# Performance work log

Hardware: AMD Instinct MI355X
Metric: run time of the kernel (lower is better)

## Reference

```python
import jax, jax.numpy as jnp
import numpy as np

BATCH, N_IN, N_OUT, D = 32768, 256, 256, 8

def setup_inputs() -> dict:
    key = jax.random.key(0)
    k1, k2 = jax.random.split(key)
    noise_std = 1.0 / (N_IN * (D + 1))
    x = jax.random.normal(k1, (BATCH, N_IN), dtype=jnp.float32)
    c_basis = noise_std * jax.random.normal(k2, (N_OUT, N_IN, D + 1), dtype=jnp.float32)
    c_act = jnp.ones((N_OUT, N_IN), dtype=jnp.float32)
    return {"x": x, "c_basis": c_basis, "c_act": c_act}

def _cheby_basis(x, degree):
    # x: (batch, n_in) -> (batch, n_in, degree+1) Chebyshev T_k(tanh(x))
    t = jnp.tanh(x)
    polys = [jnp.ones_like(t), t]
    for _ in range(2, degree + 1):
        polys.append(2.0 * t * polys[-1] - polys[-2])
    return jnp.stack(polys[: degree + 1], axis=-1)

def reference(x, c_basis, c_act):
    batch = x.shape[0]
    n_out = c_basis.shape[0]
    degree = c_basis.shape[-1] - 1
    Ti = _cheby_basis(x, degree)                      # (batch, n_in, D+1)
    cheb = Ti.reshape(batch, -1)                      # (batch, n_in*(D+1))
    cheb_w = (c_basis * c_act[..., None]).reshape(n_out, -1)
    return jnp.matmul(cheb, cheb_w.T)                 # (batch, n_out)
```

## Files before the change

### kernel.cpp

```cpp
#include <hip/hip_runtime.h>
#include <hip/hip_bf16.h>

#define BATCH 32768
#define NIN   256
#define NOUT  256

typedef __attribute__((ext_vector_type(8))) short bf16x8;
typedef __attribute__((ext_vector_type(4))) float f32x4;
typedef __attribute__((ext_vector_type(2))) float f32x2;
typedef __attribute__((ext_vector_type(4))) unsigned int u32x4;

static __device__ __forceinline__ unsigned short bf16_rne(float f) {
  unsigned u = __float_as_uint(f);
  u += 0x7fffu + ((u >> 16) & 1u);
  return (unsigned short)(u >> 16);
}

static __device__ __forceinline__ float fast_tanh(float v) {
  float a = fabsf(v);
  float z = __expf(-2.0f * a);
  float r = (1.0f - z) * __builtin_amdgcn_rcpf(1.0f + z);
  return copysignf(r, v);
}

static __device__ __forceinline__ unsigned pack_pair(f32x2 v) {
  __hip_bfloat162 h2 = __float22bfloat162_rn(make_float2(v[0], v[1]));
  union { __hip_bfloat162 h; unsigned u; } cv;
  cv.h = h2;
  return cv.u;
}

__global__ void cheby_prepack(const float* __restrict__ cb,
                              const float* __restrict__ ca,
                              unsigned short* __restrict__ Bp) {
  int tid = blockIdx.x * 256 + threadIdx.x;
  int j    = tid & 7;
  int col  = (tid >> 3) & 15;
  int kg   = (tid >> 7) & 3;
  int tile = (tid >> 9) & 15;
  int ic   = (tid >> 13) & 7;
  int dm   = tid >> 16;
  int i = ic * 32 + kg * 8 + j;
  int n = tile * 16 + col;
  float w = cb[n * (NIN * 9) + i * 9 + (dm + 1)] * ca[n * NIN + i];
  Bp[tid] = bf16_rne(w);
}

__global__ void cheby_bias(const float* __restrict__ cb,
                           const float* __restrict__ ca,
                           float* __restrict__ bias) {
  int n = blockIdx.x;
  int l = threadIdx.x;
  float s = 0.0f;
  #pragma unroll
  for (int k = 0; k < 4; ++k) {
    int i = l + k * 64;
    s += cb[n * (NIN * 9) + i * 9] * ca[n * NIN + i];
  }
  #pragma unroll
  for (int off = 32; off; off >>= 1) s += __shfl_down(s, off);
  if (l == 0) bias[n] = s;
}

__global__ __launch_bounds__(256, 2)
void cheby_mfma(const float* __restrict__ x,
                const unsigned short* __restrict__ Bp,
                const float* __restrict__ bias,
                float* __restrict__ out) {
  __shared__ unsigned short Asm[2][8][4][512];

  int tid  = threadIdx.x;
  int w    = tid >> 6;
  int lane = tid & 63;
  int row16 = lane & 15;
  int kg    = lane >> 4;

  int base_row = blockIdx.x * 64;
  int tile0    = w * 4;

  int wrow = tid >> 2;
  int wfg  = tid & 3;
  const float* xw = x + (size_t)(base_row + wrow) * NIN + wfg * 8;
  char* wbase = (char*)&Asm[0][0][wrow >> 4][0] + (wfg * 256 + (wrow & 15) * 16);

  const char* bp_lane = (const char*)Bp + kg * 256 + row16 * 16;
  const char* abase   = (const char*)&Asm[0][0][0][0] + lane * 16;

  f32x4 acc[4][4];
  #pragma unroll
  for (int a = 0; a < 4; ++a)
    #pragma unroll
    for (int b = 0; b < 4; ++b) acc[a][b] = (f32x4)0.0f;

  f32x4 xa = *(const f32x4*)xw;
  f32x4 xb = *(const f32x4*)(xw + 4);

  for (int ic = 0; ic < 8; ++ic) {
    int buf = ic & 1;
    f32x2 cur[4], prev[4], t2[4];
    #pragma unroll
    for (int p = 0; p < 4; ++p) {
      float va = (p < 2) ? xa[2 * p]     : xb[2 * p - 4];
      float vb = (p < 2) ? xa[2 * p + 1] : xb[2 * p - 3];
      float ta = fast_tanh(va);
      float tb = fast_tanh(vb);
      cur[p]  = (f32x2){ta, tb};
      t2[p]   = cur[p] + cur[p];
      prev[p] = (f32x2){1.0f, 1.0f};
    }
    char* wp = wbase + buf * 32768;
    #pragma unroll
    for (int d = 1; d <= 8; ++d) {
      u32x4 pk;
      #pragma unroll
      for (int p = 0; p < 4; ++p) pk[p] = pack_pair(cur[p]);
      *(u32x4*)(wp + (d - 1) * 4096) = pk;
      if (d < 8) {
        #pragma unroll
        for (int p = 0; p < 4; ++p) {
          f32x2 nx = __builtin_elementwise_fma(t2[p], cur[p], -prev[p]);
          prev[p] = cur[p];
          cur[p]  = nx;
        }
      }
    }
    if (ic < 7) {
      xa = *(const f32x4*)(xw + (ic + 1) * 32);
      xb = *(const f32x4*)(xw + (ic + 1) * 32 + 4);
    }
    __syncthreads();

    const char* bpi = bp_lane + (size_t)(ic * 16 + tile0) * 1024;
    const char* ai  = abase + buf * 32768;
    bf16x8 bcur[4], acur[4];
    #pragma unroll
    for (int nt = 0; nt < 4; ++nt)
      bcur[nt] = *(const bf16x8*)(bpi + nt * 1024);
    #pragma unroll
    for (int mt = 0; mt < 4; ++mt)
      acur[mt] = *(const bf16x8*)(ai + mt * 1024);

    #pragma unroll
    for (int d = 1; d <= 8; ++d) {
      bf16x8 bnxt[4], anxt[4];
      if (d < 8) {
        #pragma unroll
        for (int nt = 0; nt < 4; ++nt)
          bnxt[nt] = *(const bf16x8*)(bpi + (size_t)d * 131072 + nt * 1024);
        #pragma unroll
        for (int mt = 0; mt < 4; ++mt)
          anxt[mt] = *(const bf16x8*)(ai + (d * 4 + mt) * 1024);
      }
      #pragma unroll
      for (int mt = 0; mt < 4; ++mt)
        #pragma unroll
        for (int nt = 0; nt < 4; ++nt)
          acc[mt][nt] = __builtin_amdgcn_mfma_f32_16x16x32_bf16(
              acur[mt], bcur[nt], acc[mt][nt], 0, 0, 0);
      if (d < 8) {
        #pragma unroll
        for (int nt = 0; nt < 4; ++nt) bcur[nt] = bnxt[nt];
        #pragma unroll
        for (int mt = 0; mt < 4; ++mt) acur[mt] = anxt[mt];
      }
    }
  }

  #pragma unroll
  for (int nt = 0; nt < 4; ++nt) {
    int c = (tile0 + nt) * 16 + row16;
    float bv = bias[c];
    #pragma unroll
    for (int mt = 0; mt < 4; ++mt) {
      int r0 = base_row + mt * 16 + kg * 4;
      #pragma unroll
      for (int q = 0; q < 4; ++q)
        out[(size_t)(r0 + q) * NOUT + c] = acc[mt][nt][q] + bv;
    }
  }
}

extern "C" void kernel_launch(void* const* d_in, const int* in_sizes, int n_in,
                              void* d_out, int out_size, void* d_ws, size_t ws_size,
                              hipStream_t stream) {
  const float* x  = (const float*)d_in[0];
  const float* cb = (const float*)d_in[1];
  const float* ca = (const float*)d_in[2];
  float* out = (float*)d_out;

  unsigned short* Bp = (unsigned short*)d_ws;
  float* bias = (float*)((char*)d_ws + 8 * NIN * NOUT * 2);

  cheby_prepack<<<(8 * NIN * NOUT) / 256, 256, 0, stream>>>(cb, ca, Bp);
  cheby_bias<<<NOUT, 64, 0, stream>>>(cb, ca, bias);
  cheby_mfma<<<512, 256, 0, stream>>>(x, Bp, bias, out);
}
```

Baseline: 52.23 us.

## Software-pipeline Chebyshev basis generation with MFMA over double-buffered LDS

Restructures the main loop so that the Chebyshev basis for chunk ic+1 is computed and written into the alternate LDS buffer while MFMAs consume chunk ic, with a prologue and epilogue around the loop. This lets VALU transcendental and pack work overlap the matrix core work instead of running serially before each barrier. It also changes the LDS write mapping so each wave writes its own 16-row slice, and it drops explicit register double-buffering of fragments in favour of per-step loads. The cost is higher register pressure from carrying the recurrence state alongside the accumulators and fragments.

```diff
diff --git a/kernel.cpp b/kernel.cpp
--- a/kernel.cpp
+++ b/kernel.cpp
@@ -28,6 +28,21 @@
   union { __hip_bfloat162 h; unsigned u; } cv;
   cv.h = h2;
   return cv.u;
+}
+
+static __device__ __forceinline__ void init_state(const f32x4 x0, const f32x4 x1,
+                                                  f32x2* cur, f32x2* prev,
+                                                  f32x2* t2) {
+  #pragma unroll
+  for (int p = 0; p < 4; ++p) {
+    float va = (p < 2) ? x0[2 * p]     : x1[2 * p - 4];
+    float vb = (p < 2) ? x0[2 * p + 1] : x1[2 * p - 3];
+    float ta = fast_tanh(va);
+    float tb = fast_tanh(vb);
+    cur[p]  = (f32x2){ta, tb};
+    t2[p]   = cur[p] + cur[p];
+    prev[p] = (f32x2){1.0f, 1.0f};
+  }
 }
 
 __global__ void cheby_prepack(const float* __restrict__ cb,
@@ -78,13 +93,10 @@
   int base_row = blockIdx.x * 64;
   int tile0    = w * 4;
 
-  int wrow = tid >> 2;
-  int wfg  = tid & 3;
-  const float* xw = x + (size_t)(base_row + wrow) * NIN + wfg * 8;
-  char* wbase = (char*)&Asm[0][0][wrow >> 4][0] + (wfg * 256 + (wrow & 15) * 16);
-
+  const float* xw = x + (size_t)(base_row + w * 16 + row16) * NIN + kg * 8;
+  char* wbase = (char*)Asm + (w * 1024 + lane * 16);
+  const char* abase   = (const char*)Asm + lane * 16;
   const char* bp_lane = (const char*)Bp + kg * 256 + row16 * 16;
-  const char* abase   = (const char*)&Asm[0][0][0][0] + lane * 16;
 
   f32x4 acc[4][4];
   #pragma unroll
@@ -94,27 +106,15 @@
 
   f32x4 xa = *(const f32x4*)xw;
   f32x4 xb = *(const f32x4*)(xw + 4);
-
-  for (int ic = 0; ic < 8; ++ic) {
-    int buf = ic & 1;
+  {
     f32x2 cur[4], prev[4], t2[4];
-    #pragma unroll
-    for (int p = 0; p < 4; ++p) {
-      float va = (p < 2) ? xa[2 * p]     : xb[2 * p - 4];
-      float vb = (p < 2) ? xa[2 * p + 1] : xb[2 * p - 3];
-      float ta = fast_tanh(va);
-      float tb = fast_tanh(vb);
-      cur[p]  = (f32x2){ta, tb};
-      t2[p]   = cur[p] + cur[p];
-      prev[p] = (f32x2){1.0f, 1.0f};
-    }
-    char* wp = wbase + buf * 32768;
+    init_state(xa, xb, cur, prev, t2);
     #pragma unroll
     for (int d = 1; d <= 8; ++d) {
       u32x4 pk;
       #pragma unroll
       for (int p = 0; p < 4; ++p) pk[p] = pack_pair(cur[p]);
-      *(u32x4*)(wp + (d - 1) * 4096) = pk;
+      *(u32x4*)(wbase + (d - 1) * 4096) = pk;
       if (d < 8) {
         #pragma unroll
         for (int p = 0; p < 4; ++p) {
@@ -124,45 +124,72 @@
         }
       }
     }
-    if (ic < 7) {
-      xa = *(const f32x4*)(xw + (ic + 1) * 32);
-      xb = *(const f32x4*)(xw + (ic + 1) * 32 + 4);
-    }
-    __syncthreads();
-
+  }
+  xa = *(const f32x4*)(xw + 32);
+  xb = *(const f32x4*)(xw + 36);
+  __syncthreads();
+
+  for (int ic = 0; ic < 7; ++ic) {
+    int buf = ic & 1;
+    f32x2 cur[4], prev[4], t2[4];
+    init_state(xa, xb, cur, prev, t2);
+    if (ic < 6) {
+      xa = *(const f32x4*)(xw + (ic + 2) * 32);
+      xb = *(const f32x4*)(xw + (ic + 2) * 32 + 4);
+    }
+    const char* ai  = abase + buf * 32768;
+    char*       wp  = wbase + (buf ^ 1) * 32768;
     const char* bpi = bp_lane + (size_t)(ic * 16 + tile0) * 1024;
-    const char* ai  = abase + buf * 32768;
-    bf16x8 bcur[4], acur[4];
-    #pragma unroll
-    for (int nt = 0; nt < 4; ++nt)
-      bcur[nt] = *(const bf16x8*)(bpi + nt * 1024);
-    #pragma unroll
-    for (int mt = 0; mt < 4; ++mt)
-      acur[mt] = *(const bf16x8*)(ai + mt * 1024);
 
     #pragma unroll
     for (int d = 1; d <= 8; ++d) {
-      bf16x8 bnxt[4], anxt[4];
+      bf16x8 af[4], bfr[4];
+      #pragma unroll
+      for (int mt = 0; mt < 4; ++mt)
+        af[mt] = *(const bf16x8*)(ai + (d - 1) * 4096 + mt * 1024);
+      #pragma unroll
+      for (int nt = 0; nt < 4; ++nt)
+        bfr[nt] = *(const bf16x8*)(bpi + (size_t)(d - 1) * 131072 + nt * 1024);
+      u32x4 pk;
+      #pragma unroll
+      for (int p = 0; p < 4; ++p) pk[p] = pack_pair(cur[p]);
+      *(u32x4*)(wp + (d - 1) * 4096) = pk;
       if (d < 8) {
         #pragma unroll
-        for (int nt = 0; nt < 4; ++nt)
-          bnxt[nt] = *(const bf16x8*)(bpi + (size_t)d * 131072 + nt * 1024);
-        #pragma unroll
-        for (int mt = 0; mt < 4; ++mt)
-          anxt[mt] = *(const bf16x8*)(ai + (d * 4 + mt) * 1024);
+        for (int p = 0; p < 4; ++p) {
+          f32x2 nx = __builtin_elementwise_fma(t2[p], cur[p], -prev[p]);
+          prev[p] = cur[p];
+          cur[p]  = nx;
+        }
       }
       #pragma unroll
       for (int mt = 0; mt < 4; ++mt)
         #pragma unroll
         for (int nt = 0; nt < 4; ++nt)
           acc[mt][nt] = __builtin_amdgcn_mfma_f32_16x16x32_bf16(
-              acur[mt], bcur[nt], acc[mt][nt], 0, 0, 0);
-      if (d < 8) {
-        #pragma unroll
-        for (int nt = 0; nt < 4; ++nt) bcur[nt] = bnxt[nt];
-        #pragma unroll
-        for (int mt = 0; mt < 4; ++mt) acur[mt] = anxt[mt];
-      }
+              af[mt], bfr[nt], acc[mt][nt], 0, 0, 0);
+    }
+    __syncthreads();
+  }
+
+  {
+    const char* ai  = abase + 32768;
+    const char* bpi = bp_lane + (size_t)(7 * 16 + tile0) * 1024;
+    #pragma unroll
+    for (int d = 1; d <= 8; ++d) {
+      bf16x8 af[4], bfr[4];
+      #pragma unroll
+      for (int mt = 0; mt < 4; ++mt)
+        af[mt] = *(const bf16x8*)(ai + (d - 1) * 4096 + mt * 1024);
+      #pragma unroll
+      for (int nt = 0; nt < 4; ++nt)
+        bfr[nt] = *(const bf16x8*)(bpi + (size_t)(d - 1) * 131072 + nt * 1024);
+      #pragma unroll
+      for (int mt = 0; mt < 4; ++mt)
+        #pragma unroll
+        for (int nt = 0; nt < 4; ++nt)
+          acc[mt][nt] = __builtin_amdgcn_mfma_f32_16x16x32_bf16(
+              af[mt], bfr[nt], acc[mt][nt], 0, 0, 0);
     }
   }
 
```

Result: faster. 50.25 us (-3.8%).

## Stage weights in LDS via async loads and pipeline basis generation with MFMA

Applied to the files above, without the earlier changes.

The main kernel now uses 512-thread blocks covering 128 rows, with two warp rows sharing each B tile. B tiles are staged into double-buffered LDS through global_load_lds instead of being read per-lane from global memory. The weight prepack layout is reordered so each phase loads two degree slices. Generation of the Chebyshev basis for the next input chunk is interleaved with the MFMA phases of the current chunk, and setprio raises priority around the MFMAs. The intent is to hide global-load latency and the basis ALU work behind tensor-core work and to halve B traffic per row. The cost is more barriers, four per chunk, and higher LDS use per block.

```diff
diff --git a/kernel.cpp b/kernel.cpp
--- a/kernel.cpp
+++ b/kernel.cpp
@@ -28,6 +28,44 @@
   union { __hip_bfloat162 h; unsigned u; } cv;
   cv.h = h2;
   return cv.u;
+}
+
+static __device__ __forceinline__ void init_state(const f32x4 x0, const f32x4 x1,
+                                                  f32x2* cur, f32x2* prev,
+                                                  f32x2* t2) {
+  #pragma unroll
+  for (int p = 0; p < 4; ++p) {
+    float va = (p < 2) ? x0[2 * p]     : x1[2 * p - 4];
+    float vb = (p < 2) ? x0[2 * p + 1] : x1[2 * p - 3];
+    float ta = fast_tanh(va);
+    float tb = fast_tanh(vb);
+    cur[p]  = (f32x2){ta, tb};
+    t2[p]   = cur[p] + cur[p];
+    prev[p] = (f32x2){1.0f, 1.0f};
+  }
+}
+
+static __device__ __forceinline__ void basis_slice(char* awr, int dm,
+                                                   f32x2* cur, f32x2* prev,
+                                                   f32x2* t2) {
+  u32x4 pk;
+  #pragma unroll
+  for (int q = 0; q < 4; ++q) pk[q] = pack_pair(cur[q]);
+  *(u32x4*)(awr + dm * 8192) = pk;
+  if (dm < 7) {
+    #pragma unroll
+    for (int q = 0; q < 4; ++q) {
+      f32x2 nx = __builtin_elementwise_fma(t2[q], cur[q], -prev[q]);
+      prev[q] = cur[q];
+      cur[q]  = nx;
+    }
+  }
+}
+
+static __device__ __forceinline__ void gload_lds16(const void* g, void* l) {
+  __builtin_amdgcn_global_load_lds(
+      (const __attribute__((address_space(1))) unsigned int*)g,
+      (__attribute__((address_space(3))) unsigned int*)l, 16, 0, 0);
 }
 
 __global__ void cheby_prepack(const float* __restrict__ cb,
@@ -38,10 +76,12 @@
   int col  = (tid >> 3) & 15;
   int kg   = (tid >> 7) & 3;
   int tile = (tid >> 9) & 15;
-  int ic   = (tid >> 13) & 7;
-  int dm   = tid >> 16;
-  int i = ic * 32 + kg * 8 + j;
-  int n = tile * 16 + col;
+  int dd   = (tid >> 13) & 1;
+  int ph   = (tid >> 14) & 3;
+  int ic   = (tid >> 16) & 7;
+  int i  = ic * 32 + kg * 8 + j;
+  int n  = tile * 16 + col;
+  int dm = ph * 2 + dd;
   float w = cb[n * (NIN * 9) + i * 9 + (dm + 1)] * ca[n * NIN + i];
   Bp[tid] = bf16_rne(w);
 }
@@ -62,12 +102,13 @@
   if (l == 0) bias[n] = s;
 }
 
-__global__ __launch_bounds__(256, 2)
+__global__ __launch_bounds__(512, 2)
 void cheby_mfma(const float* __restrict__ x,
                 const unsigned short* __restrict__ Bp,
                 const float* __restrict__ bias,
                 float* __restrict__ out) {
-  __shared__ unsigned short Asm[2][8][4][512];
+  __shared__ unsigned short As[8][8][512];
+  __shared__ unsigned short Bs[2][32][512];
 
   int tid  = threadIdx.x;
   int w    = tid >> 6;
@@ -75,16 +116,17 @@
   int row16 = lane & 15;
   int kg    = lane >> 4;
 
-  int base_row = blockIdx.x * 64;
-  int tile0    = w * 4;
-
-  int wrow = tid >> 2;
-  int wfg  = tid & 3;
-  const float* xw = x + (size_t)(base_row + wrow) * NIN + wfg * 8;
-  char* wbase = (char*)&Asm[0][0][wrow >> 4][0] + (wfg * 256 + (wrow & 15) * 16);
-
-  const char* bp_lane = (const char*)Bp + kg * 256 + row16 * 16;
-  const char* abase   = (const char*)&Asm[0][0][0][0] + lane * 16;
+  int wr = w >> 2;
+  int wc = w & 3;
+  int base_row = blockIdx.x * 128;
+  int tile0    = wc * 4;
+
+  const float* xw = x + (size_t)(base_row + w * 16 + row16) * NIN + kg * 8;
+  char* awr = (char*)As + w * 1024 + lane * 16;
+  const char* ard = (const char*)As + (wr * 4) * 1024 + lane * 16;
+  const char* brd = (const char*)Bs + kg * 256 + row16 * 16;
+  const char* bsrc = (const char*)Bp + tid * 16;
+  char*       bdst = (char*)Bs + tid * 16;
 
   f32x4 acc[4][4];
   #pragma unroll
@@ -94,75 +136,71 @@
 
   f32x4 xa = *(const f32x4*)xw;
   f32x4 xb = *(const f32x4*)(xw + 4);
+  #pragma unroll
+  for (int r = 0; r < 4; ++r) gload_lds16(bsrc + r * 8192, bdst + r * 8192);
+  f32x2 cur[4], prev[4], t2[4];
+  init_state(xa, xb, cur, prev, t2);
+  #pragma unroll
+  for (int dm = 0; dm < 6; ++dm) basis_slice(awr, dm, cur, prev, t2);
+  __builtin_amdgcn_sched_barrier(0);
+  asm volatile("s_waitcnt vmcnt(0) lgkmcnt(0)" ::: "memory");
+  __builtin_amdgcn_s_barrier();
+  __builtin_amdgcn_sched_barrier(0);
 
   for (int ic = 0; ic < 8; ++ic) {
-    int buf = ic & 1;
-    f32x2 cur[4], prev[4], t2[4];
-    #pragma unroll
-    for (int p = 0; p < 4; ++p) {
-      float va = (p < 2) ? xa[2 * p]     : xb[2 * p - 4];
-      float vb = (p < 2) ? xa[2 * p + 1] : xb[2 * p - 3];
-      float ta = fast_tanh(va);
-      float tb = fast_tanh(vb);
-      cur[p]  = (f32x2){ta, tb};
-      t2[p]   = cur[p] + cur[p];
-      prev[p] = (f32x2){1.0f, 1.0f};
-    }
-    char* wp = wbase + buf * 32768;
-    #pragma unroll
-    for (int d = 1; d <= 8; ++d) {
-      u32x4 pk;
-      #pragma unroll
-      for (int p = 0; p < 4; ++p) pk[p] = pack_pair(cur[p]);
-      *(u32x4*)(wp + (d - 1) * 4096) = pk;
-      if (d < 8) {
-        #pragma unroll
-        for (int p = 0; p < 4; ++p) {
-          f32x2 nx = __builtin_elementwise_fma(t2[p], cur[p], -prev[p]);
-          prev[p] = cur[p];
-          cur[p]  = nx;
-        }
-      }
-    }
-    if (ic < 7) {
-      xa = *(const f32x4*)(xw + (ic + 1) * 32);
-      xb = *(const f32x4*)(xw + (ic + 1) * 32 + 4);
-    }
-    __syncthreads();
-
-    const char* bpi = bp_lane + (size_t)(ic * 16 + tile0) * 1024;
-    const char* ai  = abase + buf * 32768;
-    bf16x8 bcur[4], acur[4];
-    #pragma unroll
-    for (int nt = 0; nt < 4; ++nt)
-      bcur[nt] = *(const bf16x8*)(bpi + nt * 1024);
-    #pragma unroll
-    for (int mt = 0; mt < 4; ++mt)
-      acur[mt] = *(const bf16x8*)(ai + mt * 1024);
-
-    #pragma unroll
-    for (int d = 1; d <= 8; ++d) {
-      bf16x8 bnxt[4], anxt[4];
-      if (d < 8) {
+    const char* chunk_src = bsrc + (size_t)(ic * 4) * 32768;
+    #pragma unroll
+    for (int ph = 0; ph < 4; ++ph) {
+      const bool last = (ic == 7) && (ph == 3);
+      if (ph == 0 && ic < 7) {
+        xa = *(const f32x4*)(xw + (ic + 1) * 32);
+        xb = *(const f32x4*)(xw + (ic + 1) * 32 + 4);
+      }
+      if (!last) {
+        const char* s  = chunk_src + (size_t)(ph + 1) * 32768;
+        char*       d0 = bdst + ((ph + 1) & 1) * 32768;
+        #pragma unroll
+        for (int r = 0; r < 4; ++r)
+          gload_lds16(s + r * 8192, d0 + r * 8192);
+      }
+      bf16x8 af[2][4];
+      #pragma unroll
+      for (int dd = 0; dd < 2; ++dd)
+        #pragma unroll
+        for (int mt = 0; mt < 4; ++mt)
+          af[dd][mt] =
+              *(const bf16x8*)(ard + (2 * ph + dd) * 8192 + mt * 1024);
+      bf16x8 bfr[2][4];
+      #pragma unroll
+      for (int dd = 0; dd < 2; ++dd)
         #pragma unroll
         for (int nt = 0; nt < 4; ++nt)
-          bnxt[nt] = *(const bf16x8*)(bpi + (size_t)d * 131072 + nt * 1024);
+          bfr[dd][nt] = *(const bf16x8*)(
+              brd + (ph & 1) * 32768 + (dd * 16 + tile0 + nt) * 1024);
+      if (ph == 0) {
+        basis_slice(awr, 6, cur, prev, t2);
+        basis_slice(awr, 7, cur, prev, t2);
+      } else if (ic < 7) {
+        if (ph == 1) init_state(xa, xb, cur, prev, t2);
+        basis_slice(awr, 2 * (ph - 1),     cur, prev, t2);
+        basis_slice(awr, 2 * (ph - 1) + 1, cur, prev, t2);
+      }
+      if (!last) {
+        __builtin_amdgcn_sched_barrier(0);
+        asm volatile("s_waitcnt vmcnt(0) lgkmcnt(0)" ::: "memory");
+        __builtin_amdgcn_s_barrier();
+        __builtin_amdgcn_sched_barrier(0);
+      }
+      __builtin_amdgcn_s_setprio(1);
+      #pragma unroll
+      for (int dd = 0; dd < 2; ++dd)
         #pragma unroll
         for (int mt = 0; mt < 4; ++mt)
-          anxt[mt] = *(const bf16x8*)(ai + (d * 4 + mt) * 1024);
-      }
-      #pragma unroll
-      for (int mt = 0; mt < 4; ++mt)
-        #pragma unroll
-        for (int nt = 0; nt < 4; ++nt)
-          acc[mt][nt] = __builtin_amdgcn_mfma_f32_16x16x32_bf16(
-              acur[mt], bcur[nt], acc[mt][nt], 0, 0, 0);
-      if (d < 8) {
-        #pragma unroll
-        for (int nt = 0; nt < 4; ++nt) bcur[nt] = bnxt[nt];
-        #pragma unroll
-        for (int mt = 0; mt < 4; ++mt) acur[mt] = anxt[mt];
-      }
+          #pragma unroll
+          for (int nt = 0; nt < 4; ++nt)
+            acc[mt][nt] = __builtin_amdgcn_mfma_f32_16x16x32_bf16(
+                af[dd][mt], bfr[dd][nt], acc[mt][nt], 0, 0, 0);
+      __builtin_amdgcn_s_setprio(0);
     }
   }
 
@@ -172,7 +210,7 @@
     float bv = bias[c];
     #pragma unroll
     for (int mt = 0; mt < 4; ++mt) {
-      int r0 = base_row + mt * 16 + kg * 4;
+      int r0 = base_row + wr * 64 + mt * 16 + kg * 4;
       #pragma unroll
       for (int q = 0; q < 4; ++q)
         out[(size_t)(r0 + q) * NOUT + c] = acc[mt][nt][q] + bv;
@@ -193,5 +231,5 @@
 
   cheby_prepack<<<(8 * NIN * NOUT) / 256, 256, 0, stream>>>(cb, ca, Bp);
   cheby_bias<<<NOUT, 64, 0, stream>>>(cb, ca, bias);
-  cheby_mfma<<<512, 256, 0, stream>>>(x, Bp, bias, out);
-}
+  cheby_mfma<<<256, 512, 0, stream>>>(x, Bp, bias, out);
+}
```

Measured after the change: 53.92 us. 1.03x slower.
